# Performance work log

Measured on AMD Instinct MI355X. Metric: run time of the kernel, lower is better.

The kernel has to match this reference:

```python
import jax, jax.numpy as jnp
import numpy as np

B, S, D = 2, 2048, 1024
H = 16
HD = D // H
SCALE = HD ** (-0.5)


def setup_inputs() -> dict:
    key = jax.random.key(0)
    k1, k2, k3, k4 = jax.random.split(key, 4)
    x = jax.random.normal(k1, (B, S, D), dtype=jnp.float32)
    # nn.Linear-style init scale to keep activations sane
    w_qkv = jax.random.normal(k2, (3 * D, D), dtype=jnp.float32) * (D ** -0.5)
    w_out = jax.random.normal(k3, (D, D), dtype=jnp.float32) * (D ** -0.5)
    b_out = jax.random.normal(k4, (D,), dtype=jnp.float32) * 0.01
    return {"x": x, "w_qkv": w_qkv, "w_out": w_out, "b_out": b_out}


def reference(x, w_qkv, w_out, b_out):
    b, s, d = x.shape
    # qkv projection (no bias): [b, s, 3d]
    qkv = jnp.einsum('bsd,ed->bse', x, w_qkv)
    # Rearrange 'b c (e h hd) -> e b h c hd'
    qkv = qkv.reshape(b, s, 3, H, HD).transpose(2, 0, 3, 1, 4)
    # NOTE: original splits as (v, q, k) in that order
    v, q, k = qkv[0], qkv[1], qkv[2]
    # scale applied after matmul, as in the original
    scores = jnp.einsum('bhqd,bhkd->bhqk', q, k) * SCALE
    attn = jax.nn.softmax(scores, axis=-1)
    o = jnp.einsum('bhqk,bhkd->bhqd', attn, v)
    # 'b h c hd -> b c (h hd)'
    o = o.transpose(0, 2, 1, 3).reshape(b, s, d)
    return jnp.einsum('bsd,ed->bse', o, w_out) + b_out
```

## Files before the change

### kernel.cpp

```cpp
#include <hip/hip_runtime.h>
#include <cstdint>
#include <cstddef>

#define BB 2
#define SS 2048
#define DD 1024
#define HH 16
#define HDIM 64

typedef short bf16x8 __attribute__((ext_vector_type(8)));
typedef short bf16x4 __attribute__((ext_vector_type(4)));
typedef float f32x4 __attribute__((ext_vector_type(4)));
typedef float f32x2 __attribute__((ext_vector_type(2)));

union U4S8 { uint4 u; bf16x8 s; };
union U2S4 { uint2 u; bf16x4 s; unsigned short h[4]; };

#if defined(__HIP_DEVICE_COMPILE__)
# if __has_builtin(__builtin_amdgcn_exp2f)
#  define EXP2(x) __builtin_amdgcn_exp2f(x)
# else
#  define EXP2(x) exp2f(x)
# endif
#else
# define EXP2(x) exp2f(x)
#endif

__device__ __forceinline__ unsigned short f2bf(float f) {
    union { float f; unsigned int u; } c; c.f = f;
    unsigned int u = c.u;
    unsigned int r = (u + 0x7FFFu + ((u >> 16) & 1u)) >> 16;
    return (unsigned short)r;
}

__device__ __forceinline__ void async_cp16(const void* g, void* l) {
    __builtin_amdgcn_global_load_lds(
        (const __attribute__((address_space(1))) void*)g,
        (__attribute__((address_space(3))) void*)l, 16, 0, 0);
}

__global__ __launch_bounds__(256) void cvt_all(
    const float* __restrict__ x, const float* __restrict__ wq,
    const float* __restrict__ wo,
    unsigned short* __restrict__ xb, unsigned short* __restrict__ wqb,
    unsigned short* __restrict__ wob) {
    int i = blockIdx.x * 256 + threadIdx.x;
    const float* in; unsigned short* out; int j;
    if (i < 524288)       { in = x;  out = xb;  j = i; }
    else if (i < 917504)  { in = wq; out = wqb; j = i - 524288; }
    else                  { in = wo; out = wob; j = i - 917504; }
    float4 a = ((const float4*)in)[2 * j];
    float4 b = ((const float4*)in)[2 * j + 1];
    union { uint4 u; unsigned short h[8]; } o;
    o.h[0] = f2bf(a.x); o.h[1] = f2bf(a.y); o.h[2] = f2bf(a.z); o.h[3] = f2bf(a.w);
    o.h[4] = f2bf(b.x); o.h[5] = f2bf(b.y); o.h[6] = f2bf(b.z); o.h[7] = f2bf(b.w);
    ((uint4*)out)[j] = o.u;
}

__global__ __launch_bounds__(256) void gemm_qkv(
    const unsigned short* __restrict__ A,
    const unsigned short* __restrict__ Bw,
    unsigned short* __restrict__ qb, unsigned short* __restrict__ kb,
    unsigned short* __restrict__ vb) {
    const int K = 1024;
    __shared__ unsigned short smem[18432];
    int tid = threadIdx.x;
    int lane = tid & 63, wave = tid >> 6;
    int wm = (wave & 1) * 64, wn = (wave >> 1) * 64;
    int m0 = blockIdx.y * 128, n0 = blockIdx.x * 128;
    int lm = lane & 15, lq = lane >> 4;

    f32x4 acc[4][4] = {};

    int sdst = tid * 8;
    int lch = (tid & 3) ^ ((tid >> 3) & 3);
    const unsigned short* gA = A  + (size_t)(m0 + (tid >> 2)) * K + lch * 8;
    const unsigned short* gB = Bw + (size_t)(n0 + (tid >> 2)) * K + lch * 8;
    int sw = (lq ^ ((lm >> 1) & 3)) * 8;

#define GSTAGE(k0, buf) do {                                          \
        async_cp16(gA + (k0),          smem + (buf) + sdst);          \
        async_cp16(gA + 64 * K + (k0), smem + (buf) + 2048 + sdst);   \
        async_cp16(gB + (k0),          smem + (buf) + 4096 + sdst);   \
        async_cp16(gB + 64 * K + (k0), smem + (buf) + 6144 + sdst);   \
    } while (0)

    GSTAGE(0, 0);
    for (int k0 = 0; k0 < K; k0 += 64) {
        #pragma unroll
        for (int hf = 0; hf < 2; hf++) {
            int base = hf ? 8192 : 0;
            int obuf = hf ? 0 : 8192;
            __syncthreads();
            int kn = k0 + 32 + hf * 32;
            if (kn < K) GSTAGE(kn, obuf);
            const unsigned short* As = smem + base;
            const unsigned short* Bs = smem + base + 4096;
            U4S8 af[4], bfx[4];
            #pragma unroll
            for (int i = 0; i < 4; i++) {
                af[i].u  = *(const uint4*)(As + (wm + i * 16 + lm) * 32 + sw);
                bfx[i].u = *(const uint4*)(Bs + (wn + i * 16 + lm) * 32 + sw);
            }
            #pragma unroll
            for (int mi = 0; mi < 4; mi++)
                #pragma unroll
                for (int ni = 0; ni < 4; ni++)
                    acc[mi][ni] = __builtin_amdgcn_mfma_f32_16x16x32_bf16(
                        af[mi].s, bfx[ni].s, acc[mi][ni], 0, 0, 0);
        }
    }
#undef GSTAGE
    __syncthreads();

    unsigned short* Lw = smem + wave * 4608;
    int b = m0 >> 11;
    int s_base = (m0 + wm) & 2047;
    if (n0 < 1024) {
        int h = (n0 + wn) >> 6;
        #pragma unroll
        for (int mi = 0; mi < 4; mi++)
            #pragma unroll
            for (int ni = 0; ni < 4; ni++) {
                U2S4 t;
                #pragma unroll
                for (int r = 0; r < 4; r++)
                    t.h[r] = f2bf(acc[mi][ni][r]);
                *(uint2*)&Lw[(ni * 16 + lm) * 72 + mi * 16 + lq * 4] = t.u;
            }
        __builtin_amdgcn_wave_barrier();
        unsigned short* vdst = vb + ((size_t)(b * HH + h) * HDIM) * SS + s_base;
        #pragma unroll
        for (int it = 0; it < 8; it++) {
            int hd = it * 8 + (lane >> 3);
            int so = (lane & 7) * 8;
            uint4 val = *(const uint4*)&Lw[hd * 72 + so];
            *(uint4*)(vdst + (size_t)hd * SS + so) = val;
        }
    } else {
        bool isq = n0 < 2048;
        unsigned short* dst = isq ? qb : kb;
        float scale = isq ? 0.18033688f : 1.0f;
        int h = ((n0 + wn) >> 6) & 15;
        #pragma unroll
        for (int mi = 0; mi < 4; mi++)
            #pragma unroll
            for (int ni = 0; ni < 4; ni++)
                #pragma unroll
                for (int r = 0; r < 4; r++)
                    Lw[(mi * 16 + lq * 4 + r) * 72 + ni * 16 + lm] =
                        f2bf(acc[mi][ni][r] * scale);
        __builtin_amdgcn_wave_barrier();
        unsigned short* qdst =
            dst + ((size_t)(b * HH + h) * SS + s_base) * HDIM;
        #pragma unroll
        for (int it = 0; it < 8; it++) {
            int srw = it * 8 + (lane >> 3);
            int so = (lane & 7) * 8;
            uint4 val = *(const uint4*)&Lw[srw * 72 + so];
            *(uint4*)(qdst + (size_t)srw * HDIM + so) = val;
        }
    }
}

__global__ __launch_bounds__(512) void attn(
    const unsigned short* __restrict__ qb,
    const unsigned short* __restrict__ kb,
    const unsigned short* __restrict__ vb,
    unsigned short* __restrict__ ob) {
    int bh = blockIdx.y;
    int q0 = blockIdx.x * 128;
    int tid = threadIdx.x, lane = tid & 63, wave = tid >> 6;
    int grp = wave >> 2;
    int w4  = wave & 3;
    int lm = lane & 15, lq = lane >> 4;

    __shared__ unsigned short smem[32768];
    float* smf = (float*)smem;

    const unsigned short* qg = qb + (size_t)bh * SS * HDIM;
    const unsigned short* kg = kb + (size_t)bh * SS * HDIM;
    const unsigned short* vg = vb + (size_t)bh * HDIM * SS;

    U4S8 qf[2][2];
    #pragma unroll
    for (int qt = 0; qt < 2; qt++)
        #pragma unroll
        for (int ks = 0; ks < 2; ks++)
            qf[qt][ks].u = *(const uint4*)(
                qg + (size_t)(q0 + w4 * 32 + qt * 16 + lm) * HDIM + ks * 32 + lq * 8);

    f32x4 oacc[4][2] = {};
    f32x2 lsum2[2] = {};

    int lm7 = lm & 7;
    int kidx = lm * 64 + 8 * (lq ^ lm7);
    int vidx[2];
    #pragma unroll
    for (int kblk = 0; kblk < 2; kblk++)
        vidx[kblk] = lm * 64 + 8 * (((kblk << 2) | lq) ^ lm7);

    int sr  = tid >> 3;
    int s5  = sr & 31;
    int kap = (sr & 32) + (((s5 >> 2) & 3) << 3) + (((s5 >> 4) & 1) << 2) + (s5 & 3);
    int lch = (tid & 7) ^ (sr & 7);
    int sdst = tid * 8;
    const unsigned short* kpA = kg + (size_t)kap * HDIM + lch * 8;
    const unsigned short* kpB = kpA + 64 * HDIM;
    const unsigned short* vpA = vg + (size_t)sr * SS + lch * 8;
    const unsigned short* vpB = vpA + 64;

    #define STAGE(pbase)                                                       \
        do {                                                                   \
            async_cp16(kpA, smem + (pbase) + sdst);                            \
            async_cp16(kpB, smem + (pbase) + 4096 + sdst);                     \
            async_cp16(vpA, smem + (pbase) + 8192 + sdst);                     \
            async_cp16(vpB, smem + (pbase) + 12288 + sdst);                    \
            kpA += 128 * HDIM; kpB += 128 * HDIM; vpA += 128; vpB += 128;      \
        } while (0)

    STAGE(0);

    for (int kt = 0; kt < SS / 128; kt += 2) {
        #pragma unroll
        for (int hf = 0; hf < 2; hf++) {
            int cbase = hf ? 16384 : 0;
            int obase = hf ? 0 : 16384;
            __syncthreads();
            STAGE(obase);

            int kbase = cbase + grp * 4096;
            int vbase = cbase + 8192 + grp * 4096;

            U4S8 pb8[2][2];
            #pragma unroll
            for (int mi = 0; mi < 4; mi++) {
                U4S8 kf0, kf1;
                kf0.u = *(const uint4*)(smem + kbase + mi * 1024 + kidx);
                kf1.u = *(const uint4*)(smem + kbase + mi * 1024 + (kidx ^ 32));
                #pragma unroll
                for (int qt = 0; qt < 2; qt++) {
                    f32x4 sa = {};
                    sa = __builtin_amdgcn_mfma_f32_16x16x32_bf16(kf0.s, qf[qt][0].s, sa, 0, 0, 0);
                    sa = __builtin_amdgcn_mfma_f32_16x16x32_bf16(kf1.s, qf[qt][1].s, sa, 0, 0, 0);
                    float p0 = EXP2(sa[0]);
                    float p1 = EXP2(sa[1]);
                    float p2 = EXP2(sa[2]);
                    float p3 = EXP2(sa[3]);
                    f32x2 a01; a01[0] = p0; a01[1] = p1;
                    f32x2 a23; a23[0] = p2; a23[1] = p3;
                    lsum2[qt] += a01;
                    lsum2[qt] += a23;
                    unsigned int b0 = __float_as_uint(p0) + 0x8000u;
                    unsigned int b1 = __float_as_uint(p1) + 0x8000u;
                    unsigned int b2 = __float_as_uint(p2) + 0x8000u;
                    unsigned int b3 = __float_as_uint(p3) + 0x8000u;
                    unsigned int lo = __builtin_amdgcn_perm(b1, b0, 0x07060302u);
                    unsigned int hi = __builtin_amdgcn_perm(b3, b2, 0x07060302u);
                    if ((mi & 1) == 0) { pb8[mi >> 1][qt].u.x = lo; pb8[mi >> 1][qt].u.y = hi; }
                    else               { pb8[mi >> 1][qt].u.z = lo; pb8[mi >> 1][qt].u.w = hi; }
                }
            }

            #pragma unroll
            for (int mi2 = 0; mi2 < 4; mi2++) {
                #pragma unroll
                for (int kblk = 0; kblk < 2; kblk++) {
                    U4S8 vf;
                    vf.u = *(const uint4*)(smem + vbase + mi2 * 1024 + vidx[kblk]);
                    oacc[mi2][0] = __builtin_amdgcn_mfma_f32_16x16x32_bf16(
                        vf.s, pb8[kblk][0].s, oacc[mi2][0], 0, 0, 0);
                    oacc[mi2][1] = __builtin_amdgcn_mfma_f32_16x16x32_bf16(
                        vf.s, pb8[kblk][1].s, oacc[mi2][1], 0, 0, 0);
                }
            }
        }
    }
    #undef STAGE

    float gsum[2];
    #pragma unroll
    for (int qt = 0; qt < 2; qt++) {
        float s = lsum2[qt][0] + lsum2[qt][1];
        s += __shfl_xor(s, 16);
        s += __shfl_xor(s, 32);
        gsum[qt] = s;
    }

    __syncthreads();

    if (grp == 1) {
        float* pub = smf + w4 * 2048;
        #pragma unroll
        for (int mi2 = 0; mi2 < 4; mi2++)
            #pragma unroll
            for (int qt = 0; qt < 2; qt++)
                #pragma unroll
                for (int r = 0; r < 4; r++)
                    pub[(mi2 * 8 + qt * 4 + r) * 64 + lane] = oacc[mi2][qt][r];
        if (lq == 0) {
            smf[8192 + w4 * 32 + lm]      = gsum[0];
            smf[8192 + w4 * 32 + 16 + lm] = gsum[1];
        }
    }
    __syncthreads();

    if (grp == 0) {
        float* pub = smf + w4 * 2048;
        #pragma unroll
        for (int mi2 = 0; mi2 < 4; mi2++)
            #pragma unroll
            for (int qt = 0; qt < 2; qt++)
                #pragma unroll
                for (int r = 0; r < 4; r++)
                    oacc[mi2][qt][r] += pub[(mi2 * 8 + qt * 4 + r) * 64 + lane];
        float inv[2];
        inv[0] = 1.f / (gsum[0] + smf[8192 + w4 * 32 + lm]);
        inv[1] = 1.f / (gsum[1] + smf[8192 + w4 * 32 + 16 + lm]);

        unsigned short* Ow = smem + 17024 + w4 * 2304;
        #pragma unroll
        for (int mi2 = 0; mi2 < 4; mi2++)
            #pragma unroll
            for (int qt = 0; qt < 2; qt++) {
                U2S4 t;
                #pragma unroll
                for (int r = 0; r < 4; r++)
                    t.h[r] = f2bf(oacc[mi2][qt][r] * inv[qt]);
                *(uint2*)&Ow[(qt * 16 + lm) * 72 + mi2 * 16 + lq * 4] = t.u;
            }
        __builtin_amdgcn_wave_barrier();
        int b = bh >> 4, h = bh & 15;
        #pragma unroll
        for (int it = 0; it < 4; it++) {
            int q  = it * 8 + (lane >> 3);
            int off = (lane & 7) * 8;
            uint4 val = *(const uint4*)&Ow[q * 72 + off];
            int srw = q0 + w4 * 32 + q;
            *(uint4*)(ob + (size_t)(b * SS + srw) * DD + h * 64 + off) = val;
        }
    }
}

__global__ __launch_bounds__(256) void gemm_out(
    const unsigned short* __restrict__ A,
    const unsigned short* __restrict__ Bw,
    const float* __restrict__ bias, float* __restrict__ out) {
    const int K = 1024;
    __shared__ unsigned short smem[24576];
    int tid = threadIdx.x;
    int lane = tid & 63, wave = tid >> 6;
    int wm = (wave & 1) * 64, wn = (wave >> 1) * 32;
    int m0 = blockIdx.y * 128, n0 = blockIdx.x * 64;
    int lm = lane & 15, lq = lane >> 4;

    f32x4 acc[4][2] = {};

    int sdst = tid * 8;
    int lch = (tid & 3) ^ ((tid >> 3) & 3);
    const unsigned short* gA = A  + (size_t)(m0 + (tid >> 2)) * K + lch * 8;
    const unsigned short* gB = Bw + (size_t)(n0 + (tid >> 2)) * K + lch * 8;
    int sw = (lq ^ ((lm >> 1) & 3)) * 8;

#define OSTAGE(k0, buf) do {                                               \
        async_cp16(gA + (k0),               smem + (buf) + sdst);          \
        async_cp16(gA + 64 * K + (k0),      smem + (buf) + 2048 + sdst);   \
        async_cp16(gA + (k0) + 32,          smem + (buf) + 4096 + sdst);   \
        async_cp16(gA + 64 * K + (k0) + 32, smem + (buf) + 6144 + sdst);   \
        async_cp16(gB + (k0),               smem + (buf) + 8192 + sdst);   \
        async_cp16(gB + (k0) + 32,          smem + (buf) + 10240 + sdst);  \
    } while (0)

    OSTAGE(0, 0);
    for (int k0 = 0; k0 < K; k0 += 128) {
        #pragma unroll
        for (int hf = 0; hf < 2; hf++) {
            int base = hf ? 12288 : 0;
            int obuf = hf ? 0 : 12288;
            __syncthreads();
            int kn = k0 + 64 + hf * 64;
            if (kn < K) OSTAGE(kn, obuf);
            #pragma unroll
            for (int kc = 0; kc < 2; kc++) {
                const unsigned short* As = smem + base + kc * 4096;
                const unsigned short* Bs = smem + base + 8192 + kc * 2048;
                U4S8 af[4], bfx[2];
                #pragma unroll
                for (int i = 0; i < 4; i++)
                    af[i].u = *(const uint4*)(As + (wm + i * 16 + lm) * 32 + sw);
                #pragma unroll
                for (int i = 0; i < 2; i++)
                    bfx[i].u = *(const uint4*)(Bs + (wn + i * 16 + lm) * 32 + sw);
                #pragma unroll
                for (int mi = 0; mi < 4; mi++)
                    #pragma unroll
                    for (int ni = 0; ni < 2; ni++)
                        acc[mi][ni] = __builtin_amdgcn_mfma_f32_16x16x32_bf16(
                            af[mi].s, bfx[ni].s, acc[mi][ni], 0, 0, 0);
            }
        }
    }
#undef OSTAGE

    #pragma unroll
    for (int mi = 0; mi < 4; mi++) {
        int gr = m0 + wm + mi * 16 + lq * 4;
        #pragma unroll
        for (int ni = 0; ni < 2; ni++) {
            int gc = n0 + wn + ni * 16 + lm;
            float bv = bias[gc];
            #pragma unroll
            for (int r = 0; r < 4; r++)
                out[(size_t)(gr + r) * DD + gc] = acc[mi][ni][r] + bv;
        }
    }
}

extern "C" void kernel_launch(void* const* d_in, const int* in_sizes, int n_in,
                              void* d_out, int out_size, void* d_ws, size_t ws_size,
                              hipStream_t stream) {
    const float* x     = (const float*)d_in[0];
    const float* w_qkv = (const float*)d_in[1];
    const float* w_out = (const float*)d_in[2];
    const float* b_out = (const float*)d_in[3];
    float* out = (float*)d_out;

    unsigned short* ws = (unsigned short*)d_ws;
    const size_t NX = (size_t)BB * SS * DD;
    unsigned short* x_bf    = ws;
    unsigned short* wqkv_bf = x_bf + NX;
    unsigned short* wout_bf = wqkv_bf + 3145728;
    unsigned short* q_buf   = wout_bf + 1048576;
    unsigned short* k_buf   = q_buf + NX;
    unsigned short* v_buf   = k_buf + NX;
    unsigned short* o_buf   = v_buf + NX;

    cvt_all<<<4096, 256, 0, stream>>>(x, w_qkv, w_out, x_bf, wqkv_bf, wout_bf);
    gemm_qkv<<<dim3(24, 32), 256, 0, stream>>>(x_bf, wqkv_bf, q_buf, k_buf, v_buf);
    attn<<<dim3(16, 32), 512, 0, stream>>>(q_buf, k_buf, v_buf, o_buf);
    gemm_out<<<dim3(16, 32), 256, 0, stream>>>(o_buf, wout_bf, b_out, out);
}
```

Before: 191.7 us.

## Rewrite QKV GEMM with 256x256 tiles, 8 waves, and ping-pong LDS pipeline

New measurement: 196.3 us. 1.02x slower.

```diff
diff --git a/kernel.cpp b/kernel.cpp
--- a/kernel.cpp
+++ b/kernel.cpp
@@ -57,108 +57,193 @@
     ((uint4*)out)[j] = o.u;
 }
 
-__global__ __launch_bounds__(256) void gemm_qkv(
+__global__ __launch_bounds__(512, 2) void gemm_qkv(
     const unsigned short* __restrict__ A,
     const unsigned short* __restrict__ Bw,
     unsigned short* __restrict__ qb, unsigned short* __restrict__ kb,
     unsigned short* __restrict__ vb) {
     const int K = 1024;
-    __shared__ unsigned short smem[18432];
+    __shared__ unsigned short smem[65536];
     int tid = threadIdx.x;
     int lane = tid & 63, wave = tid >> 6;
-    int wm = (wave & 1) * 64, wn = (wave >> 1) * 64;
-    int m0 = blockIdx.y * 128, n0 = blockIdx.x * 128;
+    int wmp = wave & 1, wnp = wave >> 1;
     int lm = lane & 15, lq = lane >> 4;
-
-    f32x4 acc[4][4] = {};
-
+    int lm7 = lm & 7;
+
+    int id = blockIdx.y * 12 + blockIdx.x;
+    int swz = (id & 7) * 24 + (id >> 3);
+    int m0 = (swz / 12) * 256, n0 = (swz % 12) * 256;
+
+    f32x4 acc[8][4] = {};
+
+    int u = tid >> 3;
+    int csrc = ((tid & 7) ^ (u & 7)) * 8;
     int sdst = tid * 8;
-    int lch = (tid & 3) ^ ((tid >> 3) & 3);
-    const unsigned short* gA = A  + (size_t)(m0 + (tid >> 2)) * K + lch * 8;
-    const unsigned short* gB = Bw + (size_t)(n0 + (tid >> 2)) * K + lch * 8;
-    int sw = (lq ^ ((lm >> 1) & 3)) * 8;
-
-#define GSTAGE(k0, buf) do {                                          \
-        async_cp16(gA + (k0),          smem + (buf) + sdst);          \
-        async_cp16(gA + 64 * K + (k0), smem + (buf) + 2048 + sdst);   \
-        async_cp16(gB + (k0),          smem + (buf) + 4096 + sdst);   \
-        async_cp16(gB + 64 * K + (k0), smem + (buf) + 6144 + sdst);   \
+    const unsigned short* gA0 = A + (size_t)(m0 + 0   + u) * K + csrc;
+    const unsigned short* gA1 = A + (size_t)(m0 + 128 + u) * K + csrc;
+    const unsigned short* gA2 = A + (size_t)(m0 + 64  + u) * K + csrc;
+    const unsigned short* gA3 = A + (size_t)(m0 + 192 + u) * K + csrc;
+    int ub = ((tid >> 8) & 1) * 64, u31 = u & 31;
+    const unsigned short* gB0 = Bw + (size_t)(n0 + 0   + ub + u31) * K + csrc;
+    const unsigned short* gB1 = Bw + (size_t)(n0 + 128 + ub + u31) * K + csrc;
+    const unsigned short* gB2 = Bw + (size_t)(n0 + 32  + ub + u31) * K + csrc;
+    const unsigned short* gB3 = Bw + (size_t)(n0 + 160 + ub + u31) * K + csrc;
+
+#define SA0(tb, kk) async_cp16(gA0 + (kk), smem + (tb) + 0     + sdst)
+#define SA1(tb, kk) async_cp16(gA1 + (kk), smem + (tb) + 4096  + sdst)
+#define SA2(tb, kk) async_cp16(gA2 + (kk), smem + (tb) + 8192  + sdst)
+#define SA3(tb, kk) async_cp16(gA3 + (kk), smem + (tb) + 12288 + sdst)
+#define SB0(tb, kk) async_cp16(gB0 + (kk), smem + (tb) + 16384 + sdst)
+#define SB1(tb, kk) async_cp16(gB1 + (kk), smem + (tb) + 20480 + sdst)
+#define SB2(tb, kk) async_cp16(gB2 + (kk), smem + (tb) + 24576 + sdst)
+#define SB3(tb, kk) async_cp16(gB3 + (kk), smem + (tb) + 28672 + sdst)
+
+    int aBase = wmp * 4096 + lm * 64;
+    int bBase = wnp * 2048 + lm * 64;
+    int axk0 = (lq ^ lm7) * 8;
+    int axk1 = ((4 | lq) ^ lm7) * 8;
+    U4S8 af[4][2], bfr[2][2];
+
+#define LDA(cb, mh) do { _Pragma("unroll") for (int m = 0; m < 4; m++) {            \
+        af[m][0].u = *(const uint4*)(smem + (cb) + (mh) * 8192 + aBase + m * 1024 + axk0); \
+        af[m][1].u = *(const uint4*)(smem + (cb) + (mh) * 8192 + aBase + m * 1024 + axk1); \
+    } } while (0)
+#define LDB(cb, nh) do { _Pragma("unroll") for (int n = 0; n < 2; n++) {            \
+        bfr[n][0].u = *(const uint4*)(smem + (cb) + 16384 + (nh) * 8192 + bBase + n * 1024 + axk0); \
+        bfr[n][1].u = *(const uint4*)(smem + (cb) + 16384 + (nh) * 8192 + bBase + n * 1024 + axk1); \
+    } } while (0)
+#define MM(mh, nh) do { _Pragma("unroll") for (int m = 0; m < 4; m++)               \
+        _Pragma("unroll") for (int n = 0; n < 2; n++) {                             \
+            acc[(mh) * 4 + m][(nh) * 2 + n] = __builtin_amdgcn_mfma_f32_16x16x32_bf16( \
+                af[m][0].s, bfr[n][0].s, acc[(mh) * 4 + m][(nh) * 2 + n], 0, 0, 0); \
+            acc[(mh) * 4 + m][(nh) * 2 + n] = __builtin_amdgcn_mfma_f32_16x16x32_bf16( \
+                af[m][1].s, bfr[n][1].s, acc[(mh) * 4 + m][(nh) * 2 + n], 0, 0, 0); \
+        } } while (0)
+
+#define KTILE(cb, tb, kk)                                                     \
+    do {                                                                      \
+                                  \
+        LDA(cb, 0); LDB(cb, 0);                                               \
+        SA0(tb, kk); SA1(tb, kk);                                             \
+        asm volatile("s_waitcnt lgkmcnt(8)" ::: "memory");                    \
+        __builtin_amdgcn_s_barrier();                                         \
+        asm volatile("s_waitcnt lgkmcnt(0)" ::: "memory");                    \
+        __builtin_amdgcn_s_setprio(1);                                        \
+        MM(0, 0);                                                             \
+        __builtin_amdgcn_s_setprio(0);                                        \
+        asm volatile("s_waitcnt vmcnt(4)" ::: "memory");                      \
+        __builtin_amdgcn_s_barrier();                                         \
+                                 \
+        LDA(cb, 1);                                                           \
+        SB0(tb, kk); SB1(tb, kk);                                             \
+        __builtin_amdgcn_s_barrier();                                         \
+        asm volatile("s_waitcnt lgkmcnt(0)" ::: "memory");                    \
+        __builtin_amdgcn_s_setprio(1);                                        \
+        MM(1, 0);                                                             \
+        __builtin_amdgcn_s_setprio(0);                                        \
+        asm volatile("s_waitcnt vmcnt(4)" ::: "memory");                      \
+        __builtin_amdgcn_s_barrier();                                         \
+                                 \
+        LDB(cb, 1);                                                           \
+        SA2(tb, kk); SA3(tb, kk);                                             \
+        __builtin_amdgcn_s_barrier();                                         \
+        asm volatile("s_waitcnt lgkmcnt(0)" ::: "memory");                    \
+        __builtin_amdgcn_s_setprio(1);                                        \
+        MM(1, 1);                                                             \
+        __builtin_amdgcn_s_setprio(0);                                        \
+        __builtin_amdgcn_s_barrier();                                         \
+                         \
+        LDA(cb, 0);                                                           \
+        SB2(tb, kk); SB3(tb, kk);                                             \
+        __builtin_amdgcn_s_barrier();                                         \
+        asm volatile("s_waitcnt lgkmcnt(0)" ::: "memory");                    \
+        __builtin_amdgcn_s_setprio(1);                                        \
+        MM(0, 1);                                                             \
+        __builtin_amdgcn_s_setprio(0);                                        \
+        asm volatile("s_waitcnt vmcnt(4)" ::: "memory");                      \
+        __builtin_amdgcn_s_barrier();                                         \
     } while (0)
 
-    GSTAGE(0, 0);
-    for (int k0 = 0; k0 < K; k0 += 64) {
-        #pragma unroll
-        for (int hf = 0; hf < 2; hf++) {
-            int base = hf ? 8192 : 0;
-            int obuf = hf ? 0 : 8192;
-            __syncthreads();
-            int kn = k0 + 32 + hf * 32;
-            if (kn < K) GSTAGE(kn, obuf);
-            const unsigned short* As = smem + base;
-            const unsigned short* Bs = smem + base + 4096;
-            U4S8 af[4], bfx[4];
-            #pragma unroll
-            for (int i = 0; i < 4; i++) {
-                af[i].u  = *(const uint4*)(As + (wm + i * 16 + lm) * 32 + sw);
-                bfx[i].u = *(const uint4*)(Bs + (wn + i * 16 + lm) * 32 + sw);
-            }
-            #pragma unroll
-            for (int mi = 0; mi < 4; mi++)
-                #pragma unroll
-                for (int ni = 0; ni < 4; ni++)
-                    acc[mi][ni] = __builtin_amdgcn_mfma_f32_16x16x32_bf16(
-                        af[mi].s, bfx[ni].s, acc[mi][ni], 0, 0, 0);
-        }
-    }
-#undef GSTAGE
-    __syncthreads();
-
-    unsigned short* Lw = smem + wave * 4608;
+    SA0(0, 0); SA1(0, 0); SB0(0, 0); SB1(0, 0);
+    SA2(0, 0); SA3(0, 0); SB2(0, 0); SB3(0, 0);
+    asm volatile("s_waitcnt vmcnt(4)" ::: "memory");
+    __builtin_amdgcn_s_barrier();
+
+    #pragma unroll 1
+    for (int t2 = 0; t2 < 8; ++t2) {
+        int kk = t2 * 128;
+        KTILE(0, 32768, kk + 64);
+        KTILE(32768, 0, kk + 128);
+    }
+#undef KTILE
+#undef MM
+#undef LDB
+#undef LDA
+#undef SA0
+#undef SA1
+#undef SA2
+#undef SA3
+#undef SB0
+#undef SB1
+#undef SB2
+#undef SB3
+
+    asm volatile("s_waitcnt vmcnt(0)" ::: "memory");
+    __builtin_amdgcn_s_barrier();
+
+    unsigned short* Lw = smem + wave * 8192;
+    int wm = wmp * 128, wn = wnp * 64;
     int b = m0 >> 11;
     int s_base = (m0 + wm) & 2047;
+    int h = ((n0 + wn) >> 6) & 15;
     if (n0 < 1024) {
-        int h = (n0 + wn) >> 6;
-        #pragma unroll
-        for (int mi = 0; mi < 4; mi++)
-            #pragma unroll
-            for (int ni = 0; ni < 4; ni++) {
-                U2S4 t;
-                #pragma unroll
-                for (int r = 0; r < 4; r++)
-                    t.h[r] = f2bf(acc[mi][ni][r]);
-                *(uint2*)&Lw[(ni * 16 + lm) * 72 + mi * 16 + lq * 4] = t.u;
+        unsigned short* vdst = vb + ((size_t)(b * HH + h) * HDIM) * SS;
+        #pragma unroll
+        for (int c = 0; c < 2; c++) {
+            #pragma unroll
+            for (int m4 = 0; m4 < 4; m4++)
+                #pragma unroll
+                for (int ni = 0; ni < 4; ni++) {
+                    U2S4 t;
+                    #pragma unroll
+                    for (int r = 0; r < 4; r++)
+                        t.h[r] = f2bf(acc[c * 4 + m4][ni][r]);
+                    *(uint2*)&Lw[(ni * 16 + lm) * 72 + m4 * 16 + lq * 4] = t.u;
+                }
+            __builtin_amdgcn_wave_barrier();
+            #pragma unroll
+            for (int it = 0; it < 8; it++) {
+                int hd = it * 8 + (lane >> 3);
+                int so = (lane & 7) * 8;
+                uint4 val = *(const uint4*)&Lw[hd * 72 + so];
+                *(uint4*)(vdst + (size_t)hd * SS + s_base + c * 64 + so) = val;
             }
-        __builtin_amdgcn_wave_barrier();
-        unsigned short* vdst = vb + ((size_t)(b * HH + h) * HDIM) * SS + s_base;
-        #pragma unroll
-        for (int it = 0; it < 8; it++) {
-            int hd = it * 8 + (lane >> 3);
-            int so = (lane & 7) * 8;
-            uint4 val = *(const uint4*)&Lw[hd * 72 + so];
-            *(uint4*)(vdst + (size_t)hd * SS + so) = val;
+            __builtin_amdgcn_wave_barrier();
         }
     } else {
         bool isq = n0 < 2048;
         unsigned short* dst = isq ? qb : kb;
         float scale = isq ? 0.18033688f : 1.0f;
-        int h = ((n0 + wn) >> 6) & 15;
-        #pragma unroll
-        for (int mi = 0; mi < 4; mi++)
-            #pragma unroll
-            for (int ni = 0; ni < 4; ni++)
-                #pragma unroll
-                for (int r = 0; r < 4; r++)
-                    Lw[(mi * 16 + lq * 4 + r) * 72 + ni * 16 + lm] =
-                        f2bf(acc[mi][ni][r] * scale);
-        __builtin_amdgcn_wave_barrier();
-        unsigned short* qdst =
-            dst + ((size_t)(b * HH + h) * SS + s_base) * HDIM;
-        #pragma unroll
-        for (int it = 0; it < 8; it++) {
-            int srw = it * 8 + (lane >> 3);
-            int so = (lane & 7) * 8;
-            uint4 val = *(const uint4*)&Lw[srw * 72 + so];
-            *(uint4*)(qdst + (size_t)srw * HDIM + so) = val;
+        unsigned short* qdst = dst + ((size_t)(b * HH + h) * SS) * HDIM;
+        #pragma unroll
+        for (int c = 0; c < 2; c++) {
+            #pragma unroll
+            for (int m4 = 0; m4 < 4; m4++)
+                #pragma unroll
+                for (int ni = 0; ni < 4; ni++)
+                    #pragma unroll
+                    for (int r = 0; r < 4; r++)
+                        Lw[(m4 * 16 + lq * 4 + r) * 72 + ni * 16 + lm] =
+                            f2bf(acc[c * 4 + m4][ni][r] * scale);
+            __builtin_amdgcn_wave_barrier();
+            #pragma unroll
+            for (int it = 0; it < 8; it++) {
+                int srw = it * 8 + (lane >> 3);
+                int so = (lane & 7) * 8;
+                uint4 val = *(const uint4*)&Lw[srw * 72 + so];
+                *(uint4*)(qdst + (size_t)(s_base + c * 64 + srw) * HDIM + so) = val;
+            }
+            __builtin_amdgcn_wave_barrier();
         }
     }
 }
@@ -436,7 +521,7 @@
     unsigned short* o_buf   = v_buf + NX;
 
     cvt_all<<<4096, 256, 0, stream>>>(x, w_qkv, w_out, x_bf, wqkv_bf, wout_bf);
-    gemm_qkv<<<dim3(24, 32), 256, 0, stream>>>(x_bf, wqkv_bf, q_buf, k_buf, v_buf);
+    gemm_qkv<<<dim3(12, 16), 512, 0, stream>>>(x_bf, wqkv_bf, q_buf, k_buf, v_buf);
     attn<<<dim3(16, 32), 512, 0, stream>>>(q_buf, k_buf, v_buf, o_buf);
     gemm_out<<<dim3(16, 32), 256, 0, stream>>>(o_buf, wout_bf, b_out, out);
 }
```

## Enlarge QKV GEMM tiles to 256x256 with 4-stage async pipeline and block swizzle

Applied to the files above, without the earlier changes.

Measured after the change: 178.6 us. 1.07x faster.

```diff
diff --git a/kernel.cpp b/kernel.cpp
--- a/kernel.cpp
+++ b/kernel.cpp
@@ -57,108 +57,133 @@
     ((uint4*)out)[j] = o.u;
 }
 
-__global__ __launch_bounds__(256) void gemm_qkv(
+__global__ __launch_bounds__(512, 2) void gemm_qkv(
     const unsigned short* __restrict__ A,
     const unsigned short* __restrict__ Bw,
     unsigned short* __restrict__ qb, unsigned short* __restrict__ kb,
     unsigned short* __restrict__ vb) {
     const int K = 1024;
-    __shared__ unsigned short smem[18432];
+    __shared__ unsigned short smem[65536];
     int tid = threadIdx.x;
     int lane = tid & 63, wave = tid >> 6;
-    int wm = (wave & 1) * 64, wn = (wave >> 1) * 64;
-    int m0 = blockIdx.y * 128, n0 = blockIdx.x * 128;
+    int wmp = wave & 1, wnp = wave >> 1;
     int lm = lane & 15, lq = lane >> 4;
 
-    f32x4 acc[4][4] = {};
-
+    int id = blockIdx.y * 12 + blockIdx.x;
+    int swz = (id & 7) * 24 + (id >> 3);
+    int m0 = (swz / 12) * 256, n0 = (swz % 12) * 256;
+
+    f32x4 acc[8][4] = {};
+
+    int u2 = tid >> 2;
+    int c2 = (tid & 3) ^ (u2 & 3);
     int sdst = tid * 8;
-    int lch = (tid & 3) ^ ((tid >> 3) & 3);
-    const unsigned short* gA = A  + (size_t)(m0 + (tid >> 2)) * K + lch * 8;
-    const unsigned short* gB = Bw + (size_t)(n0 + (tid >> 2)) * K + lch * 8;
-    int sw = (lq ^ ((lm >> 1) & 3)) * 8;
-
-#define GSTAGE(k0, buf) do {                                          \
-        async_cp16(gA + (k0),          smem + (buf) + sdst);          \
-        async_cp16(gA + 64 * K + (k0), smem + (buf) + 2048 + sdst);   \
-        async_cp16(gB + (k0),          smem + (buf) + 4096 + sdst);   \
-        async_cp16(gB + 64 * K + (k0), smem + (buf) + 6144 + sdst);   \
+    const unsigned short* gA0 = A  + (size_t)(m0 + u2) * K + c2 * 8;
+    const unsigned short* gB0 = Bw + (size_t)(n0 + u2) * K + c2 * 8;
+    const unsigned short* gA1 = gA0 + (size_t)128 * K;
+    const unsigned short* gB1 = gB0 + (size_t)128 * K;
+
+#define STAGE4(j, kk) do {                                                  \
+        async_cp16(gA0 + (kk), smem + (j) * 16384 + 0     + sdst);          \
+        async_cp16(gA1 + (kk), smem + (j) * 16384 + 4096  + sdst);          \
+        async_cp16(gB0 + (kk), smem + (j) * 16384 + 8192  + sdst);          \
+        async_cp16(gB1 + (kk), smem + (j) * 16384 + 12288 + sdst);          \
     } while (0)
 
-    GSTAGE(0, 0);
-    for (int k0 = 0; k0 < K; k0 += 64) {
-        #pragma unroll
-        for (int hf = 0; hf < 2; hf++) {
-            int base = hf ? 8192 : 0;
-            int obuf = hf ? 0 : 8192;
-            __syncthreads();
-            int kn = k0 + 32 + hf * 32;
-            if (kn < K) GSTAGE(kn, obuf);
-            const unsigned short* As = smem + base;
-            const unsigned short* Bs = smem + base + 4096;
-            U4S8 af[4], bfx[4];
-            #pragma unroll
-            for (int i = 0; i < 4; i++) {
-                af[i].u  = *(const uint4*)(As + (wm + i * 16 + lm) * 32 + sw);
-                bfx[i].u = *(const uint4*)(Bs + (wn + i * 16 + lm) * 32 + sw);
-            }
-            #pragma unroll
-            for (int mi = 0; mi < 4; mi++)
-                #pragma unroll
-                for (int ni = 0; ni < 4; ni++)
-                    acc[mi][ni] = __builtin_amdgcn_mfma_f32_16x16x32_bf16(
-                        af[mi].s, bfx[ni].s, acc[mi][ni], 0, 0, 0);
-        }
-    }
-#undef GSTAGE
-    __syncthreads();
-
-    unsigned short* Lw = smem + wave * 4608;
+    int axk = (lq ^ (lm & 3)) * 8;
+    int aBase = (wmp * 128 + lm) * 32 + axk;
+    int bBase = 8192 + (wnp * 64 + lm) * 32 + axk;
+    U4S8 af[8], bfr[4];
+
+#define KT(j, kk3) do {                                                     \
+        _Pragma("unroll")                                                   \
+        for (int m = 0; m < 8; m++)                                         \
+            af[m].u = *(const uint4*)(smem + (j) * 16384 + aBase + m * 512);\
+        _Pragma("unroll")                                                   \
+        for (int n = 0; n < 4; n++)                                         \
+            bfr[n].u = *(const uint4*)(smem + (j) * 16384 + bBase + n * 512);\
+        STAGE4((((j) + 3) & 3), kk3);                                       \
+        _Pragma("unroll")                                                   \
+        for (int m = 0; m < 8; m++)                                         \
+            _Pragma("unroll")                                               \
+            for (int n = 0; n < 4; n++)                                     \
+                acc[m][n] = __builtin_amdgcn_mfma_f32_16x16x32_bf16(        \
+                    af[m].s, bfr[n].s, acc[m][n], 0, 0, 0);                 \
+        asm volatile("s_waitcnt vmcnt(8)" ::: "memory");                    \
+        __builtin_amdgcn_s_barrier();                                       \
+    } while (0)
+
+    STAGE4(0, 0); STAGE4(1, 32); STAGE4(2, 64);
+    asm volatile("s_waitcnt vmcnt(8)" ::: "memory");
+    __builtin_amdgcn_s_barrier();
+
+    #pragma unroll 1
+    for (int t4 = 0; t4 < 8; ++t4) {
+        int kb128 = t4 * 128;
+        KT(0, kb128 + 96);
+        KT(1, kb128 + 128);
+        KT(2, kb128 + 160);
+        KT(3, kb128 + 192);
+    }
+#undef KT
+#undef STAGE4
+
+    asm volatile("s_waitcnt vmcnt(0)" ::: "memory");
+    __builtin_amdgcn_s_barrier();
+
+    unsigned short* Lw = smem + wave * 8192;
+    int wm = wmp * 128, wn = wnp * 64;
     int b = m0 >> 11;
     int s_base = (m0 + wm) & 2047;
+    int h = ((n0 + wn) >> 6) & 15;
     if (n0 < 1024) {
-        int h = (n0 + wn) >> 6;
-        #pragma unroll
-        for (int mi = 0; mi < 4; mi++)
-            #pragma unroll
-            for (int ni = 0; ni < 4; ni++) {
-                U2S4 t;
-                #pragma unroll
-                for (int r = 0; r < 4; r++)
-                    t.h[r] = f2bf(acc[mi][ni][r]);
-                *(uint2*)&Lw[(ni * 16 + lm) * 72 + mi * 16 + lq * 4] = t.u;
-            }
-        __builtin_amdgcn_wave_barrier();
-        unsigned short* vdst = vb + ((size_t)(b * HH + h) * HDIM) * SS + s_base;
-        #pragma unroll
-        for (int it = 0; it < 8; it++) {
-            int hd = it * 8 + (lane >> 3);
-            int so = (lane & 7) * 8;
-            uint4 val = *(const uint4*)&Lw[hd * 72 + so];
-            *(uint4*)(vdst + (size_t)hd * SS + so) = val;
+        unsigned short* vdst = vb + ((size_t)(b * HH + h) * HDIM) * SS;
+        #pragma unroll
+        for (int c = 0; c < 2; c++) {
+            #pragma unroll
+            for (int m4 = 0; m4 < 4; m4++)
+                #pragma unroll
+                for (int ni = 0; ni < 4; ni++) {
+                    U2S4 t;
+                    #pragma unroll
+                    for (int r = 0; r < 4; r++)
+                        t.h[r] = f2bf(acc[c * 4 + m4][ni][r]);
+                    *(uint2*)&Lw[(ni * 16 + lm) * 72 + m4 * 16 + lq * 4] = t.u;
+                }
+            __builtin_amdgcn_wave_barrier();
+            #pragma unroll
+            for (int it = 0; it < 8; it++) {
+                int hd = it * 8 + (lane >> 3);
+                int so = (lane & 7) * 8;
+                uint4 val = *(const uint4*)&Lw[hd * 72 + so];
+                *(uint4*)(vdst + (size_t)hd * SS + s_base + c * 64 + so) = val;
+            }
+            __builtin_amdgcn_wave_barrier();
         }
     } else {
         bool isq = n0 < 2048;
         unsigned short* dst = isq ? qb : kb;
         float scale = isq ? 0.18033688f : 1.0f;
-        int h = ((n0 + wn) >> 6) & 15;
-        #pragma unroll
-        for (int mi = 0; mi < 4; mi++)
-            #pragma unroll
-            for (int ni = 0; ni < 4; ni++)
-                #pragma unroll
-                for (int r = 0; r < 4; r++)
-                    Lw[(mi * 16 + lq * 4 + r) * 72 + ni * 16 + lm] =
-                        f2bf(acc[mi][ni][r] * scale);
-        __builtin_amdgcn_wave_barrier();
-        unsigned short* qdst =
-            dst + ((size_t)(b * HH + h) * SS + s_base) * HDIM;
-        #pragma unroll
-        for (int it = 0; it < 8; it++) {
-            int srw = it * 8 + (lane >> 3);
-            int so = (lane & 7) * 8;
-            uint4 val = *(const uint4*)&Lw[srw * 72 + so];
-            *(uint4*)(qdst + (size_t)srw * HDIM + so) = val;
+        unsigned short* qdst = dst + ((size_t)(b * HH + h) * SS) * HDIM;
+        #pragma unroll
+        for (int c = 0; c < 2; c++) {
+            #pragma unroll
+            for (int m4 = 0; m4 < 4; m4++)
+                #pragma unroll
+                for (int ni = 0; ni < 4; ni++)
+                    #pragma unroll
+                    for (int r = 0; r < 4; r++)
+                        Lw[(m4 * 16 + lq * 4 + r) * 72 + ni * 16 + lm] =
+                            f2bf(acc[c * 4 + m4][ni][r] * scale);
+            __builtin_amdgcn_wave_barrier();
+            #pragma unroll
+            for (int it = 0; it < 8; it++) {
+                int srw = it * 8 + (lane >> 3);
+                int so = (lane & 7) * 8;
+                uint4 val = *(const uint4*)&Lw[srw * 72 + so];
+                *(uint4*)(qdst + (size_t)(s_base + c * 64 + srw) * HDIM + so) = val;
+            }
+            __builtin_amdgcn_wave_barrier();
         }
     }
 }
@@ -436,7 +461,7 @@
     unsigned short* o_buf   = v_buf + NX;
 
     cvt_all<<<4096, 256, 0, stream>>>(x, w_qkv, w_out, x_bf, wqkv_bf, wout_bf);
-    gemm_qkv<<<dim3(24, 32), 256, 0, stream>>>(x_bf, wqkv_bf, q_buf, k_buf, v_buf);
+    gemm_qkv<<<dim3(12, 16), 512, 0, stream>>>(x_bf, wqkv_bf, q_buf, k_buf, v_buf);
     attn<<<dim3(16, 32), 512, 0, stream>>>(q_buf, k_buf, v_buf, o_buf);
     gemm_out<<<dim3(16, 32), 256, 0, stream>>>(o_buf, wout_bf, b_out, out);
 }
```
